# Kernel optimization log

Measured on AMD Instinct MI355X. Metric: run time of the kernel, lower is better.

The kernel has to match this reference:

```python
import jax, jax.numpy as jnp
import numpy as np


def setup_inputs() -> dict:
    key = jax.random.key(0)
    k1, k2 = jax.random.split(key)
    x = jax.random.normal(k1, (8, 2048, 512), dtype=jnp.float32)
    # codebook, init std=0.001 as in the torch module
    weight = jax.random.normal(k2, (8192, 512), dtype=jnp.float32) * 0.001
    return {"x": x, "weight": weight}


def reference(x, weight):
    """x: (*, E), weight: (Q, E) -> (quantized (*, E), idx (*,)).

    Same math as torch: dist[n,q] = sum_e (w[q,e] - x[n,e])**2, argmin over q,
    gather codebook rows. Uses the ||x||^2 - 2 x.w + ||w||^2 expansion so only
    the (N, Q) distance matrix is materialized (not the (N, Q, E) delta).
    """
    in_shape = x.shape
    E = weight.shape[1]
    xf = x.reshape(-1, E)                                  # (N, E)
    x_sq = jnp.sum(xf * xf, axis=-1, keepdims=True)        # (N, 1)
    w_sq = jnp.sum(weight * weight, axis=-1)               # (Q,)
    dist = x_sq - 2.0 * jnp.einsum("ne,qe->nq", xf, weight) + w_sq[None, :]
    q_idx = jnp.argmin(dist, axis=-1)                      # (N,)
    q_data = weight[q_idx]                                 # (N, E)
    return q_data.reshape(in_shape), q_idx.reshape(in_shape[:-1])
```

## Files before the change

### kernel.cpp

```cpp
#include <hip/hip_runtime.h>
#include <stdint.h>

#define NROWS 16384
#define QNUM  8192
#define ED    512
#define BM    128
#define BN    128
#define KTILES 8
#define QBLKS  (QNUM / BN)
#define DELTA  0.02f
#define ESLOT  17

typedef long  l2    __attribute__((ext_vector_type(2)));
typedef float f32x4 __attribute__((ext_vector_type(4)));

static __device__ __forceinline__ unsigned enc_key(float s, unsigned idx) {
    const unsigned b = __float_as_uint(s);
    const unsigned m = (unsigned)(((int)b) >> 31) | 0x80000000u;
    return ((b ^ m) & 0xFFFFE000u) | idx;
}
static __device__ __forceinline__ float dec_key(unsigned k) {
    const unsigned u = k & 0xFFFFE000u;
    return (u & 0x80000000u) ? __uint_as_float(u ^ 0x80000000u)
                             : __uint_as_float(~u);
}

static __device__ __forceinline__ void ins3k(unsigned& v1, unsigned& v2, unsigned& v3,
                                             unsigned k) {
    const bool b1 = k < v1, b2 = k < v2, b3 = k < v3;
    v3 = b2 ? v2 : (b3 ? k : v3);
    v2 = b1 ? v1 : (b2 ? k : v2);
    v1 = b1 ? k : v1;
}

#define SROWS 32
#define SSTRIDE 520
__global__ __launch_bounds__(256) void k_prep_sumsq(const float* __restrict__ src,
                                                    float* __restrict__ dst_sq,
                                                    unsigned long long* __restrict__ dst8,
                                                    float scale) {
    __shared__ float ld[SROWS * SSTRIDE];
    const int t = threadIdx.x;
    const size_t base = (size_t)blockIdx.x * SROWS * ED;
    #pragma unroll
    for (int k = 0; k < 16; ++k) {
        int u = k * 256 + t;
        int row = u >> 7;
        int c4  = u & 127;
        float4 v = ((const float4*)(src + base))[u];
        float* d = ld + row * SSTRIDE + c4 * 4;
        d[0] = v.x; d[1] = v.y; d[2] = v.z; d[3] = v.w;
    }
    __syncthreads();
    const int row = t >> 3, j = t & 7;
    const float* a = ld + row * SSTRIDE;
    float B[4];
    #pragma unroll
    for (int b = 0; b < 4; ++b) {
        const float* p = a + b * 128 + j;
        float r = __fmul_rn(p[0], p[0]);
        #pragma unroll
        for (int i = 1; i < 16; ++i) {
            float q = p[8 * i];
            r = __fadd_rn(r, __fmul_rn(q, q));
        }
        float t1 = __fadd_rn(r,  __shfl_xor(r,  1, 64));
        float t2 = __fadd_rn(t1, __shfl_xor(t1, 2, 64));
        B[b]     = __fadd_rn(t2, __shfl_xor(t2, 4, 64));
    }
    if (j == 0)
        dst_sq[(size_t)blockIdx.x * SROWS + row] =
            __fadd_rn(__fadd_rn(B[0], B[1]), __fadd_rn(B[2], B[3]));

    const int gr = blockIdx.x * SROWS + row;
    const int rt = gr >> 4, cc = gr & 15;
    #pragma unroll
    for (int gi = 0; gi < 8; ++gi) {
        const float* e = a + (j * 8 + gi) * 8;
        int lo = __builtin_amdgcn_cvt_pk_fp8_f32(e[0] * scale, e[1] * scale, 0, false);
        lo     = __builtin_amdgcn_cvt_pk_fp8_f32(e[2] * scale, e[3] * scale, lo, true);
        int hi = __builtin_amdgcn_cvt_pk_fp8_f32(e[4] * scale, e[5] * scale, 0, false);
        hi     = __builtin_amdgcn_cvt_pk_fp8_f32(e[6] * scale, e[7] * scale, hi, true);
        const unsigned long long v = (unsigned)lo | ((unsigned long long)(unsigned)hi << 32);
        const int g = gi & 3, half = gi >> 2;
        dst8[((size_t)(rt * 8 + j) * 64 + g * 16 + cc) * 2 + half] = v;
    }
}

__global__ __launch_bounds__(256, 2) void k_gemm_top2(
        const l2* __restrict__ xb,
        const l2* __restrict__ wb,
        const float* __restrict__ wsqf,
        uint4* __restrict__ p3) {
    __shared__ uint2 ered[BM * ESLOT];

    const int t  = threadIdx.x;
    const int wv = t >> 6;
    const int l  = t & 63;
    const int c  = l & 15;
    const int g  = l >> 4;
    const int RB = (wv >> 1) * 64;
    const int CB = (wv & 1) * 64;

    const int id = blockIdx.x;
    const int qb = (id & 7) * 8 + ((id >> 3) & 7);
    const int rb = id >> 6;
    const int q0 = qb * BN;
    const int r0 = rb * BM;

    f32x4 acc[4][4];
    #pragma unroll
    for (int i = 0; i < 4; ++i)
        #pragma unroll
        for (int j = 0; j < 4; ++j)
            acc[i][j] = (f32x4){0.f, 0.f, 0.f, 0.f};

    const l2* ga = xb + ((size_t)((r0 + RB) >> 4) * 8) * 64 + l;
    const l2* gb = wb + ((size_t)((q0 + CB) >> 4) * 8) * 64 + l;

    l2 Af[2][4], Bf[2][4];

    #pragma unroll
    for (int i = 0; i < 4; ++i) Af[0][i] = ga[(size_t)(i * 8) * 64];
    #pragma unroll
    for (int j = 0; j < 4; ++j) Bf[0][j] = gb[(size_t)(j * 8) * 64];

    #pragma unroll
    for (int kt = 0; kt < KTILES; ++kt) {
        const int cur = kt & 1, nxt = cur ^ 1;
        if (kt + 1 < KTILES) {
            #pragma unroll
            for (int i = 0; i < 4; ++i) Af[nxt][i] = ga[(size_t)(i * 8 + kt + 1) * 64];
            #pragma unroll
            for (int j = 0; j < 4; ++j) Bf[nxt][j] = gb[(size_t)(j * 8 + kt + 1) * 64];
        }
        #pragma unroll
        for (int s = 0; s < 2; ++s)
            #pragma unroll
            for (int i = 0; i < 4; ++i)
                #pragma unroll
                for (int j = 0; j < 4; ++j) {
                    const long a8 = s ? Af[cur][i].y : Af[cur][i].x;
                    const long b8 = s ? Bf[cur][j].y : Bf[cur][j].x;
                    acc[i][j] = __builtin_amdgcn_mfma_f32_16x16x32_fp8_fp8(a8, b8, acc[i][j], 0, 0, 0);
                }
    }

    float wsqv[4]; unsigned kidx[4];
    #pragma unroll
    for (int j = 0; j < 4; ++j) {
        const int qj = q0 + CB + j * 16 + c;
        wsqv[j] = wsqf[qj];
        kidx[j] = (unsigned)qj;
    }

    #pragma unroll
    for (int i = 0; i < 4; ++i) {
        #pragma unroll
        for (int r = 0; r < 4; ++r) {
            unsigned k0 = enc_key(fmaf(-0.00390625f, acc[i][0][r], wsqv[0]), kidx[0]);
            unsigned k1 = enc_key(fmaf(-0.00390625f, acc[i][1][r], wsqv[1]), kidx[1]);
            unsigned k2 = enc_key(fmaf(-0.00390625f, acc[i][2][r], wsqv[2]), kidx[2]);
            unsigned k3 = enc_key(fmaf(-0.00390625f, acc[i][3][r], wsqv[3]), kidx[3]);
            const unsigned a01 = min(k0, k1), b01 = max(k0, k1);
            const unsigned a23 = min(k2, k3), b23 = max(k2, k3);
            unsigned v1 = min(a01, a23);
            unsigned v2 = min(min(max(a01, a23), b01), b23);
            const unsigned o1 = __shfl_xor((int)v1, 8, 64);
            const unsigned o2 = __shfl_xor((int)v2, 8, 64);
            const unsigned nv1 = min(v1, o1);
            v2 = min(min(max(v1, o1), v2), o2);
            v1 = nv1;
            if (c < 8) {
                const int row = RB + i * 16 + g * 4 + r;
                ered[row * ESLOT + (wv & 1) * 8 + c] = make_uint2(v1, v2);
            }
        }
    }
    __syncthreads();
    if (t < BM) {
        const uint2* e = &ered[t * ESLOT];
        unsigned v1 = 0xFFFFFFFFu, v2 = 0xFFFFFFFFu, v3 = 0xFFFFFFFFu;
        #pragma unroll
        for (int k = 0; k < 16; ++k) {
            const uint2 E = e[k];
            ins3k(v1, v2, v3, E.x);
            ins3k(v1, v2, v3, E.y);
        }
        p3[(size_t)(r0 + t) * QBLKS + qb] = make_uint4(v1, v2, v3, 0xFFFFFFFFu);
    }
}

__global__ __launch_bounds__(256) void k_rescore(
        const uint4* __restrict__ p3,
        const float* __restrict__ x,
        const float* __restrict__ wt,
        const float* __restrict__ wsqf,
        const float* __restrict__ xsqf,
        float* __restrict__ outq,
        float* __restrict__ outi) {
    const int wv = threadIdx.x >> 6, l = threadIdx.x & 63;
    const int row = blockIdx.x * 4 + wv;

    const uint4 P = p3[(size_t)row * QBLKS + l];
    unsigned vk[3] = { P.x, P.y, P.z };

    unsigned gk = vk[0];
    #pragma unroll
    for (int m = 1; m < 64; m <<= 1) gk = min(gk, (unsigned)__shfl_xor((int)gk, m, 64));
    const float tf = dec_key(gk) + DELTA;
    const unsigned tb = __float_as_uint(tf);
    const unsigned tm = (unsigned)(((int)tb) >> 31) | 0x80000000u;
    const unsigned thrkey = (tb ^ tm) | 0x1FFFu;

    const float4* xp = (const float4*)(x + (size_t)row * ED + l * 8);
    const float4 xa = xp[0], xbv = xp[1];
    const float xsq = xsqf[row];

    float bestv = 3.4e38f; int bestq = 0x7fffffff;
    #pragma unroll
    for (int k = 0; k < 3; ++k) {
        unsigned long long mm = __ballot(vk[k] <= thrkey);
        while (mm) {
            const int ln = __ffsll(mm) - 1;
            mm &= mm - 1;
            const int q = __shfl((int)vk[k], ln, 64) & 0x1FFF;
            const float4* wp = (const float4*)(wt + (size_t)q * ED + l * 8);
            const float4 wa = wp[0], wbv = wp[1];
            double d = (double)xa.x * wa.x + (double)xa.y * wa.y
                     + (double)xa.z * wa.z + (double)xa.w * wa.w
                     + (double)xbv.x * wbv.x + (double)xbv.y * wbv.y
                     + (double)xbv.z * wbv.z + (double)xbv.w * wbv.w;
            #pragma unroll
            for (int m = 1; m < 64; m <<= 1) d += __shfl_xor(d, m, 64);
            const float dotf = (float)d;
            const float t1 = __fadd_rn(xsq, __fmul_rn(-2.0f, dotf));
            const float sc = __fadd_rn(t1, wsqf[q]);
            if (sc < bestv || (sc == bestv && q < bestq)) { bestv = sc; bestq = q; }
        }
    }
    const float4* wp = (const float4*)(wt + (size_t)bestq * ED + l * 8);
    float4* op = (float4*)(outq + (size_t)row * ED + l * 8);
    op[0] = wp[0]; op[1] = wp[1];
    if (l == 0) outi[row] = (float)bestq;
}

extern "C" void kernel_launch(void* const* d_in, const int* in_sizes, int n_in,
                              void* d_out, int out_size, void* d_ws, size_t ws_size,
                              hipStream_t stream) {
    (void)in_sizes; (void)n_in; (void)out_size; (void)ws_size;
    const float* x  = (const float*)d_in[0];
    const float* wt = (const float*)d_in[1];

    char* ws = (char*)d_ws;
    unsigned long long* xb8 = (unsigned long long*)ws;
    unsigned long long* wb8 = (unsigned long long*)(ws + 8388608);
    float* wsqf = (float*)(ws + 12582912);
    float* xsqf = (float*)(ws + 12615680);
    uint4* p3   = (uint4*)(ws + 12681216);

    float* outq = (float*)d_out;
    float* outi = outq + (size_t)NROWS * ED;

    k_prep_sumsq<<<NROWS / SROWS, 256, 0, stream>>>(x,  xsqf, xb8, 1.0f);
    k_prep_sumsq<<<QNUM  / SROWS, 256, 0, stream>>>(wt, wsqf, wb8, 512.0f);
    k_gemm_top2<<<8192, 256, 0, stream>>>((const l2*)xb8, (const l2*)wb8, wsqf, p3);
    k_rescore<<<4096, 256, 0, stream>>>(p3, x, wt, wsqf, xsqf, outq, outi);
}
```

Baseline: 240.8 us.

## Switch FP8 GEMM to 32x32x64 scaled MFMA with matching operand layout

Replaces the 16x16x32 fp8 MFMA tiles with the gfx950 mfma_scale 32x32x64 f8f6f4 instruction, using unit scales. The prep kernel now packs fp8 operands in a layout suited to that instruction, so each lane loads 32 bytes per tile as two 16-byte loads. The top-2 epilogue is reworked for the 32x32 accumulator lane mapping with an extra shuffle stage, and s_setprio is raised around the MFMA block. The aim is fewer, denser matrix instructions and wider loads, at the cost of a more complex layout that must exactly match the hardware operand format.

```diff
diff --git a/kernel.cpp b/kernel.cpp
--- a/kernel.cpp
+++ b/kernel.cpp
@@ -11,8 +11,8 @@
 #define DELTA  0.02f
 #define ESLOT  17
 
-typedef long  l2    __attribute__((ext_vector_type(2)));
-typedef float f32x4 __attribute__((ext_vector_type(4)));
+typedef int   i32x8  __attribute__((ext_vector_type(8)));
+typedef float f32x16 __attribute__((ext_vector_type(16)));
 
 static __device__ __forceinline__ unsigned enc_key(float s, unsigned idx) {
     const unsigned b = __float_as_uint(s);
@@ -72,24 +72,26 @@
         dst_sq[(size_t)blockIdx.x * SROWS + row] =
             __fadd_rn(__fadd_rn(B[0], B[1]), __fadd_rn(B[2], B[3]));
 
-    const int gr = blockIdx.x * SROWS + row;
-    const int rt = gr >> 4, cc = gr & 15;
-    #pragma unroll
-    for (int gi = 0; gi < 8; ++gi) {
-        const float* e = a + (j * 8 + gi) * 8;
-        int lo = __builtin_amdgcn_cvt_pk_fp8_f32(e[0] * scale, e[1] * scale, 0, false);
-        lo     = __builtin_amdgcn_cvt_pk_fp8_f32(e[2] * scale, e[3] * scale, lo, true);
-        int hi = __builtin_amdgcn_cvt_pk_fp8_f32(e[4] * scale, e[5] * scale, 0, false);
-        hi     = __builtin_amdgcn_cvt_pk_fp8_f32(e[6] * scale, e[7] * scale, hi, true);
-        const unsigned long long v = (unsigned)lo | ((unsigned long long)(unsigned)hi << 32);
-        const int g = gi & 3, half = gi >> 2;
-        dst8[((size_t)(rt * 8 + j) * 64 + g * 16 + cc) * 2 + half] = v;
+    #pragma unroll
+    for (int kb = 0; kb < 2; ++kb) {
+        const float* e = a + j * 64 + kb * 32;
+        unsigned d[8];
+        #pragma unroll
+        for (int p = 0; p < 8; ++p) {
+            int w0 = __builtin_amdgcn_cvt_pk_fp8_f32(e[4*p+0] * scale, e[4*p+1] * scale, 0,  false);
+            w0     = __builtin_amdgcn_cvt_pk_fp8_f32(e[4*p+2] * scale, e[4*p+3] * scale, w0, true);
+            d[p] = (unsigned)w0;
+        }
+        const size_t G = ((size_t)(blockIdx.x * 8 + j) * 64 + kb * 32 + row);
+        uint4* dp = (uint4*)dst8 + G * 2;
+        dp[0] = make_uint4(d[0], d[1], d[2], d[3]);
+        dp[1] = make_uint4(d[4], d[5], d[6], d[7]);
     }
 }
 
 __global__ __launch_bounds__(256, 2) void k_gemm_top2(
-        const l2* __restrict__ xb,
-        const l2* __restrict__ wb,
+        const uint4* __restrict__ xb,
+        const uint4* __restrict__ wb,
         const float* __restrict__ wsqf,
         uint4* __restrict__ p3) {
     __shared__ uint2 ered[BM * ESLOT];
@@ -97,8 +99,8 @@
     const int t  = threadIdx.x;
     const int wv = t >> 6;
     const int l  = t & 63;
-    const int c  = l & 15;
-    const int g  = l >> 4;
+    const int h  = l >> 5;
+    const int cn = l & 31;
     const int RB = (wv >> 1) * 64;
     const int CB = (wv & 1) * 64;
 
@@ -108,72 +110,93 @@
     const int q0 = qb * BN;
     const int r0 = rb * BM;
 
-    f32x4 acc[4][4];
-    #pragma unroll
-    for (int i = 0; i < 4; ++i)
-        #pragma unroll
-        for (int j = 0; j < 4; ++j)
-            acc[i][j] = (f32x4){0.f, 0.f, 0.f, 0.f};
-
-    const l2* ga = xb + ((size_t)((r0 + RB) >> 4) * 8) * 64 + l;
-    const l2* gb = wb + ((size_t)((q0 + CB) >> 4) * 8) * 64 + l;
-
-    l2 Af[2][4], Bf[2][4];
-
-    #pragma unroll
-    for (int i = 0; i < 4; ++i) Af[0][i] = ga[(size_t)(i * 8) * 64];
-    #pragma unroll
-    for (int j = 0; j < 4; ++j) Bf[0][j] = gb[(size_t)(j * 8) * 64];
+    f32x16 acc[2][2];
+    #pragma unroll
+    for (int i = 0; i < 2; ++i)
+        #pragma unroll
+        for (int j = 0; j < 2; ++j)
+            #pragma unroll
+            for (int r = 0; r < 16; ++r)
+                acc[i][j][r] = 0.f;
+
+    const int rt0 = (r0 + RB) >> 5;
+    const int qt0 = (q0 + CB) >> 5;
+    const uint4* ga = xb + ((size_t)(rt0 * 8) * 64 + l) * 2;
+    const uint4* gb = wb + ((size_t)(qt0 * 8) * 64 + l) * 2;
+
+    i32x8 Af[2][2], Bf[2][2];
+
+#define LD32(dst, p, blk) do {                                   \
+        const uint4 u0 = (p)[(size_t)(blk) * 128];               \
+        const uint4 u1 = (p)[(size_t)(blk) * 128 + 1];           \
+        dst = (i32x8){(int)u0.x, (int)u0.y, (int)u0.z, (int)u0.w,\
+                      (int)u1.x, (int)u1.y, (int)u1.z, (int)u1.w};\
+    } while (0)
+
+    #pragma unroll
+    for (int i = 0; i < 2; ++i) LD32(Af[0][i], ga, i * 8);
+    #pragma unroll
+    for (int j = 0; j < 2; ++j) LD32(Bf[0][j], gb, j * 8);
 
     #pragma unroll
     for (int kt = 0; kt < KTILES; ++kt) {
         const int cur = kt & 1, nxt = cur ^ 1;
         if (kt + 1 < KTILES) {
             #pragma unroll
-            for (int i = 0; i < 4; ++i) Af[nxt][i] = ga[(size_t)(i * 8 + kt + 1) * 64];
-            #pragma unroll
-            for (int j = 0; j < 4; ++j) Bf[nxt][j] = gb[(size_t)(j * 8 + kt + 1) * 64];
-        }
-        #pragma unroll
-        for (int s = 0; s < 2; ++s)
-            #pragma unroll
-            for (int i = 0; i < 4; ++i)
-                #pragma unroll
-                for (int j = 0; j < 4; ++j) {
-                    const long a8 = s ? Af[cur][i].y : Af[cur][i].x;
-                    const long b8 = s ? Bf[cur][j].y : Bf[cur][j].x;
-                    acc[i][j] = __builtin_amdgcn_mfma_f32_16x16x32_fp8_fp8(a8, b8, acc[i][j], 0, 0, 0);
-                }
-    }
-
-    float wsqv[4]; unsigned kidx[4];
-    #pragma unroll
-    for (int j = 0; j < 4; ++j) {
-        const int qj = q0 + CB + j * 16 + c;
+            for (int i = 0; i < 2; ++i) LD32(Af[nxt][i], ga, i * 8 + kt + 1);
+            #pragma unroll
+            for (int j = 0; j < 2; ++j) LD32(Bf[nxt][j], gb, j * 8 + kt + 1);
+        }
+        __builtin_amdgcn_s_setprio(1);
+        #pragma unroll
+        for (int i = 0; i < 2; ++i)
+            #pragma unroll
+            for (int j = 0; j < 2; ++j)
+                acc[i][j] = __builtin_amdgcn_mfma_scale_f32_32x32x64_f8f6f4(
+                        Af[cur][i], Bf[cur][j], acc[i][j],
+                        0, 0,
+                        0, 0x7F7F7F7F,
+                        0, 0x7F7F7F7F);
+        __builtin_amdgcn_s_setprio(0);
+    }
+
+    float wsqv[2]; unsigned kidx[2];
+    #pragma unroll
+    for (int j = 0; j < 2; ++j) {
+        const int qj = q0 + CB + j * 32 + cn;
         wsqv[j] = wsqf[qj];
         kidx[j] = (unsigned)qj;
     }
 
     #pragma unroll
-    for (int i = 0; i < 4; ++i) {
-        #pragma unroll
-        for (int r = 0; r < 4; ++r) {
-            unsigned k0 = enc_key(fmaf(-0.00390625f, acc[i][0][r], wsqv[0]), kidx[0]);
-            unsigned k1 = enc_key(fmaf(-0.00390625f, acc[i][1][r], wsqv[1]), kidx[1]);
-            unsigned k2 = enc_key(fmaf(-0.00390625f, acc[i][2][r], wsqv[2]), kidx[2]);
-            unsigned k3 = enc_key(fmaf(-0.00390625f, acc[i][3][r], wsqv[3]), kidx[3]);
-            const unsigned a01 = min(k0, k1), b01 = max(k0, k1);
-            const unsigned a23 = min(k2, k3), b23 = max(k2, k3);
-            unsigned v1 = min(a01, a23);
-            unsigned v2 = min(min(max(a01, a23), b01), b23);
-            const unsigned o1 = __shfl_xor((int)v1, 8, 64);
-            const unsigned o2 = __shfl_xor((int)v2, 8, 64);
-            const unsigned nv1 = min(v1, o1);
-            v2 = min(min(max(v1, o1), v2), o2);
-            v1 = nv1;
-            if (c < 8) {
-                const int row = RB + i * 16 + g * 4 + r;
-                ered[row * ESLOT + (wv & 1) * 8 + c] = make_uint2(v1, v2);
+    for (int i = 0; i < 2; ++i) {
+        #pragma unroll
+        for (int rg = 0; rg < 4; ++rg) {
+            #pragma unroll
+            for (int rr = 0; rr < 4; ++rr) {
+                const int reg = rg * 4 + rr;
+                const unsigned k0 = enc_key(fmaf(-0.00390625f, acc[i][0][reg], wsqv[0]), kidx[0]);
+                const unsigned k1 = enc_key(fmaf(-0.00390625f, acc[i][1][reg], wsqv[1]), kidx[1]);
+                unsigned v1 = min(k0, k1);
+                unsigned v2 = max(k0, k1);
+                {
+                    const unsigned o1 = __shfl_xor((int)v1, 8, 64);
+                    const unsigned o2 = __shfl_xor((int)v2, 8, 64);
+                    const unsigned nv1 = min(v1, o1);
+                    v2 = min(max(v1, o1), min(v2, o2));
+                    v1 = nv1;
+                }
+                {
+                    const unsigned o1 = __shfl_xor((int)v1, 16, 64);
+                    const unsigned o2 = __shfl_xor((int)v2, 16, 64);
+                    const unsigned nv1 = min(v1, o1);
+                    v2 = min(max(v1, o1), min(v2, o2));
+                    v1 = nv1;
+                }
+                if ((l & 24) == 0) {
+                    const int row = RB + i * 32 + rr + 8 * rg + 4 * h;
+                    ered[row * ESLOT + (wv & 1) * 8 + (l & 7)] = make_uint2(v1, v2);
+                }
             }
         }
     }
@@ -264,6 +287,6 @@
 
     k_prep_sumsq<<<NROWS / SROWS, 256, 0, stream>>>(x,  xsqf, xb8, 1.0f);
     k_prep_sumsq<<<QNUM  / SROWS, 256, 0, stream>>>(wt, wsqf, wb8, 512.0f);
-    k_gemm_top2<<<8192, 256, 0, stream>>>((const l2*)xb8, (const l2*)wb8, wsqf, p3);
+    k_gemm_top2<<<8192, 256, 0, stream>>>((const uint4*)xb8, (const uint4*)wb8, wsqf, p3);
     k_rescore<<<4096, 256, 0, stream>>>(p3, x, wt, wsqf, xsqf, outq, outi);
 }
```

Result: slower. 266.7 us (+10.8%).
